# Kernel tuning notes

Measured on AMD Instinct MI355X. Metric: run time of the kernel, lower is better.

The kernel has to match this reference:

```python
import jax, jax.numpy as jnp
import numpy as np

WINDOW_SIZES = [3, 5, 7, 9]
THETA = 1.0
INCLUDE = ['contrast', 'energy', 'entropy', 'homogeneity']
EPS = 1e-6


def _extract_patches(x, w):
    # x: [B, C, H, W] -> [B, C, K=w*w, H, W] with zero padding (matches F.unfold)
    pad = w // 2
    H, W = x.shape[2], x.shape[3]
    xp = jnp.pad(x, ((0, 0), (0, 0), (pad, pad), (pad, pad)))
    shifts = [xp[:, :, i:i + H, j:j + W] for i in range(w) for j in range(w)]
    return jnp.stack(shifts, axis=2)


def _glcm_feats(patches):
    # patches: [B, C, K, H, W]; all reductions over K (axis=2)
    mean = jnp.mean(patches, axis=2, keepdims=True)
    std = jnp.std(patches, axis=2, ddof=1, keepdims=True) + EPS  # torch.std is unbiased
    normed = (patches - mean) / std
    contrast = jnp.mean(normed ** 2, axis=2)
    energy = jnp.mean(patches ** 2, axis=2)
    entropy = -jnp.mean(patches * jnp.log(patches + EPS), axis=2)
    homogeneity = 1.0 / jnp.mean(1.0 + jnp.abs(patches - mean), axis=2)
    return {'contrast': contrast, 'energy': energy,
            'entropy': entropy, 'homogeneity': homogeneity}


def setup_inputs() -> dict:
    key = jax.random.key(0)
    x = jax.random.uniform(key, (2, 3, 512, 512), dtype=jnp.float32)
    return {'x': x}


def reference(x):
    B, C, H, W = x.shape
    per_window = []
    for w in WINDOW_SIZES:
        patches = _extract_patches(x, w)          # [B, C, K, H, W]
        feats = _glcm_feats(patches)
        Ms = []
        for name in ['contrast', 'energy', 'entropy', 'homogeneity']:
            if name in INCLUDE:
                log_feat = jnp.log(feats[name] + EPS)
                Ms.append(jnp.exp(THETA * log_feat - 0.5 * THETA ** 2))
        per_window.append(jnp.stack(Ms, axis=2))  # [B, C, F, H, W]
    out = jnp.concatenate(per_window, axis=2)     # [B, C, nW*F, H, W]
    # channel-major ordering (c outer, then window, then feature) matches the
    # torch module's per-channel loop + final cat along dim=1
    return out.reshape(B, C * out.shape[2], H, W)
```

## Files before the change

### kernel.cpp

```cpp
#include <hip/hip_runtime.h>
#include <math.h>

#define BC 6
#define H_ 512
#define W_ 512
#define HW (H_ * W_)
#define EPS 1e-6f
#define EXPM05 0.60653065971263342f

#define TW 72
#define TH 16
#define XSS 18
#define VHS 72

__global__ __launch_bounds__(256) void texmart_kernel(const float* __restrict__ x,
                                                      float* __restrict__ out) {
    __shared__ float xs[TW][XSS];
    __shared__ float vh[48][VHS];

    const int tx = threadIdx.x, ty = threadIdx.y;
    const int tid = ty * 64 + tx;
    const int bx = blockIdx.x * 64, by = blockIdx.y * 8;
    const int plane = blockIdx.z;
    const float* __restrict__ xp = x + (size_t)plane * HW;

    for (int idx = tid; idx < TW * TH; idx += 256) {
        const int t = idx / TW, c = idx - t * TW;
        const int gy = by + t - 4, gx = bx + c - 4;
        float v = 0.f;
        if (gy >= 0 && gy < H_ && gx >= 0 && gx < W_) v = xp[gy * W_ + gx];
        xs[c][t] = v;
    }
    __syncthreads();

    int uoA[3], ucA[3];
    float s1A[3], s2A[3], slA[3];
#pragma unroll
    for (int i = 0; i < 3; ++i) {
        const int u = tid + i * 256;
        const int uu = (u < 576) ? u : 0;
        const int o = uu / 72, c = uu - o * 72;
        uoA[i] = o; ucA[i] = c;
        const float pc = xs[c][o + 4];
        s1A[i] = pc;
        s2A[i] = pc * pc;
        slA[i] = pc * __logf(pc + EPS);
    }

    float mean[2][4];
    const int gxx = bx + tx;
    float* __restrict__ obase = out + (size_t)plane * 16 * HW + (size_t)by * W_ + gxx;

#pragma unroll
    for (int round = 0; round < 2; ++round) {
        const int Rb = 1 + 2 * round;

#pragma unroll
        for (int i = 0; i < 3; ++i) {
            if (i < 2 || tid < 64) {
                const int o = uoA[i], c = ucA[i];
#pragma unroll
                for (int rr = 0; rr < 2; ++rr) {
                    const int R = Rb + rr;
                    const float plo = xs[c][o + 4 - R];
                    const float phi = xs[c][o + 4 + R];
                    s1A[i] += plo + phi;
                    s2A[i] = __fmaf_rn(plo, plo, __fmaf_rn(phi, phi, s2A[i]));
                    slA[i] += plo * __logf(plo + EPS) + phi * __logf(phi + EPS);
                    vh[(rr * 3 + 0) * 8 + o][c] = s1A[i];
                    vh[(rr * 3 + 1) * 8 + o][c] = s2A[i];
                    vh[(rr * 3 + 2) * 8 + o][c] = slA[i];
                }
            }
        }
        __syncthreads();

#pragma unroll
        for (int rr = 0; rr < 2; ++rr) {
            const int R = Rb + rr;
            const float K = (float)((2 * R + 1) * (2 * R + 1));
            const float invK = 1.f / K;
            const float invKm1 = 1.f / (K - 1.f);
#pragma unroll
            for (int oi = 0; oi < 2; ++oi) {
                const int o = ty * 2 + oi;
                float S1 = 0.f, S2 = 0.f, SL = 0.f;
#pragma unroll
                for (int s = -4; s <= 4; ++s) {
                    if (s >= -R && s <= R) {
                        S1 += vh[(rr * 3 + 0) * 8 + o][tx + 4 + s];
                        S2 += vh[(rr * 3 + 1) * 8 + o][tx + 4 + s];
                        SL += vh[(rr * 3 + 2) * 8 + o][tx + 4 + s];
                    }
                }
                const float m = S1 * invK;
                mean[oi][R - 1] = m;
                float S2c = __fmaf_rn(-S1, m, S2);
                if (S2c < 0.f) S2c = 0.f;
                const float sd = sqrtf(S2c * invKm1) + EPS;
                const float contrast = (S2c * invK) * __frcp_rn(sd * sd);
                const float energy = S2 * invK;
                const float entropy = -SL * invK;

                float* __restrict__ o4 = obase + (size_t)o * W_ + (size_t)(R - 1) * 4 * HW;
                o4[0 * HW] = (contrast + EPS) * EXPM05;
                o4[1 * HW] = (energy + EPS) * EXPM05;
                o4[2 * HW] = (entropy + EPS) * EXPM05;
            }
        }
        if (round == 0) __syncthreads();
    }

    const int ty2 = ty * 2;
    float sa[2][4];
#pragma unroll
    for (int oi = 0; oi < 2; ++oi)
#pragma unroll
        for (int R = 0; R < 4; ++R) sa[oi][R] = 0.f;

#pragma unroll
    for (int dj = 0; dj < 9; ++dj) {
        const int a = dj < 4 ? 4 - dj : dj - 4;
        const float* __restrict__ col = &xs[tx + dj][ty2];
        const float2 u0 = *(const float2*)(col + 0);
        const float2 u1 = *(const float2*)(col + 2);
        const float2 u2 = *(const float2*)(col + 4);
        const float2 u3 = *(const float2*)(col + 6);
        const float2 u4 = *(const float2*)(col + 8);
        const float p[10] = {u0.x, u0.y, u1.x, u1.y, u2.x, u2.y, u3.x, u3.y, u4.x, u4.y};

#pragma unroll
        for (int oi = 0; oi < 2; ++oi) {
#pragma unroll
            for (int k = 0; k < 9; ++k) {
                const int adi = k < 4 ? 4 - k : k - 4;
                const int rm = a > adi ? a : adi;
                const int r0 = rm < 1 ? 1 : rm;
#pragma unroll
                for (int R = 1; R <= 4; ++R) {
                    if (R >= r0) sa[oi][R - 1] += fabsf(p[oi + k] - mean[oi][R - 1]);
                }
            }
        }
    }

#pragma unroll
    for (int oi = 0; oi < 2; ++oi) {
        const int o = ty2 + oi;
#pragma unroll
        for (int R = 1; R <= 4; ++R) {
            const float K = (float)((2 * R + 1) * (2 * R + 1));
            const float homog = __frcp_rn(1.f + sa[oi][R - 1] * (1.f / K));
            obase[(size_t)o * W_ + (size_t)(R - 1) * 4 * HW + 3 * HW] =
                (homog + EPS) * EXPM05;
        }
    }
}

extern "C" void kernel_launch(void* const* d_in, const int* in_sizes, int n_in,
                              void* d_out, int out_size, void* d_ws, size_t ws_size,
                              hipStream_t stream) {
    const float* x = (const float*)d_in[0];
    float* out = (float*)d_out;
    dim3 block(64, 4, 1);
    dim3 grid(W_ / 64, H_ / 8, BC);
    texmart_kernel<<<grid, block, 0, stream>>>(x, out);
}
```

Baseline: 45.52 us.

## Retile to 64x32 blocks with four-column threads, cached logs and sliding sums

Grows each block's tile from 64x8 to 64x32 and gives every thread four adjacent output columns. It precomputes x*log(x) once per tile element into shared memory, so the vertical prefix passes no longer recompute logs, and processes each radius separately with float4 shared loads. The horizontal window sums now slide across the four columns, and all outputs are written as float4 stores. In exchange, shared memory and register pressure rise (per-thread mean and abs-deviation arrays), which may reduce occupancy.

```diff
diff --git a/kernel.cpp b/kernel.cpp
--- a/kernel.cpp
+++ b/kernel.cpp
@@ -8,137 +8,159 @@
 #define EPS 1e-6f
 #define EXPM05 0.60653065971263342f
 
-#define TW 72
-#define TH 16
-#define XSS 18
-#define VHS 72
+#define TCOLS 72
+#define TROWS 40
+#define XST 76
 
 __global__ __launch_bounds__(256) void texmart_kernel(const float* __restrict__ x,
                                                       float* __restrict__ out) {
-    __shared__ float xs[TW][XSS];
-    __shared__ float vh[48][VHS];
+    __shared__ float xs[TROWS][XST];
+    __shared__ float qs[TROWS][XST];
+    __shared__ float vh[3][32][XST];
 
-    const int tx = threadIdx.x, ty = threadIdx.y;
-    const int tid = ty * 64 + tx;
-    const int bx = blockIdx.x * 64, by = blockIdx.y * 8;
+    const int tix = threadIdx.x;
+    const int tiy = threadIdx.y;
+    const int tid = tiy * 16 + tix;
+    const int bx = blockIdx.x * 64, by = blockIdx.y * 32;
     const int plane = blockIdx.z;
     const float* __restrict__ xp = x + (size_t)plane * HW;
 
-    for (int idx = tid; idx < TW * TH; idx += 256) {
-        const int t = idx / TW, c = idx - t * TW;
+    for (int idx = tid; idx < TROWS * TCOLS; idx += 256) {
+        const int t = idx / TCOLS, c = idx - t * TCOLS;
         const int gy = by + t - 4, gx = bx + c - 4;
         float v = 0.f;
         if (gy >= 0 && gy < H_ && gx >= 0 && gx < W_) v = xp[gy * W_ + gx];
-        xs[c][t] = v;
+        xs[t][c] = v;
+        qs[t][c] = v * __logf(v + EPS);
     }
     __syncthreads();
 
+    float s1A[3][4], s2A[3][4], slA[3][4];
     int uoA[3], ucA[3];
-    float s1A[3], s2A[3], slA[3];
 #pragma unroll
     for (int i = 0; i < 3; ++i) {
         const int u = tid + i * 256;
         const int uu = (u < 576) ? u : 0;
-        const int o = uu / 72, c = uu - o * 72;
-        uoA[i] = o; ucA[i] = c;
-        const float pc = xs[c][o + 4];
-        s1A[i] = pc;
-        s2A[i] = pc * pc;
-        slA[i] = pc * __logf(pc + EPS);
+        const int o = uu / 18, cg = uu - (uu / 18) * 18;
+        uoA[i] = o; ucA[i] = 4 * cg;
+        float pc[4], qc[4];
+        *(float4*)pc = *(const float4*)&xs[o + 4][4 * cg];
+        *(float4*)qc = *(const float4*)&qs[o + 4][4 * cg];
+#pragma unroll
+        for (int j = 0; j < 4; ++j) {
+            s1A[i][j] = pc[j];
+            s2A[i][j] = pc[j] * pc[j];
+            slA[i][j] = qc[j];
+        }
     }
 
-    float mean[2][4];
-    const int gxx = bx + tx;
-    float* __restrict__ obase = out + (size_t)plane * 16 * HW + (size_t)by * W_ + gxx;
+    float mean_[2][4][4];
+    const int gx0 = bx + 4 * tix;
+    float* __restrict__ obase = out + (size_t)plane * 16 * HW + (size_t)by * W_ + gx0;
 
 #pragma unroll
-    for (int round = 0; round < 2; ++round) {
-        const int Rb = 1 + 2 * round;
-
+    for (int R = 1; R <= 4; ++R) {
 #pragma unroll
         for (int i = 0; i < 3; ++i) {
             if (i < 2 || tid < 64) {
-                const int o = uoA[i], c = ucA[i];
+                const int o = uoA[i], c4 = ucA[i];
+                float lo[4], hi[4], ql[4], qh[4];
+                *(float4*)lo = *(const float4*)&xs[o + 4 - R][c4];
+                *(float4*)hi = *(const float4*)&xs[o + 4 + R][c4];
+                *(float4*)ql = *(const float4*)&qs[o + 4 - R][c4];
+                *(float4*)qh = *(const float4*)&qs[o + 4 + R][c4];
+                float w1[4], w2[4], wl[4];
 #pragma unroll
-                for (int rr = 0; rr < 2; ++rr) {
-                    const int R = Rb + rr;
-                    const float plo = xs[c][o + 4 - R];
-                    const float phi = xs[c][o + 4 + R];
-                    s1A[i] += plo + phi;
-                    s2A[i] = __fmaf_rn(plo, plo, __fmaf_rn(phi, phi, s2A[i]));
-                    slA[i] += plo * __logf(plo + EPS) + phi * __logf(phi + EPS);
-                    vh[(rr * 3 + 0) * 8 + o][c] = s1A[i];
-                    vh[(rr * 3 + 1) * 8 + o][c] = s2A[i];
-                    vh[(rr * 3 + 2) * 8 + o][c] = slA[i];
+                for (int j = 0; j < 4; ++j) {
+                    s1A[i][j] += lo[j] + hi[j];
+                    s2A[i][j] = __fmaf_rn(lo[j], lo[j], __fmaf_rn(hi[j], hi[j], s2A[i][j]));
+                    slA[i][j] += ql[j] + qh[j];
+                    w1[j] = s1A[i][j]; w2[j] = s2A[i][j]; wl[j] = slA[i][j];
                 }
+                *(float4*)&vh[0][o][c4] = *(float4*)w1;
+                *(float4*)&vh[1][o][c4] = *(float4*)w2;
+                *(float4*)&vh[2][o][c4] = *(float4*)wl;
             }
         }
         __syncthreads();
 
+        const float K = (float)((2 * R + 1) * (2 * R + 1));
+        const float invK = 1.f / K;
+        const float invKm1 = 1.f / (K - 1.f);
 #pragma unroll
-        for (int rr = 0; rr < 2; ++rr) {
-            const int R = Rb + rr;
-            const float K = (float)((2 * R + 1) * (2 * R + 1));
-            const float invK = 1.f / K;
-            const float invKm1 = 1.f / (K - 1.f);
+        for (int oi = 0; oi < 2; ++oi) {
+            const int o = 2 * tiy + oi;
+            float v1[12], v2[12], vl[12];
+            *(float4*)&v1[0] = *(const float4*)&vh[0][o][4 * tix + 0];
+            *(float4*)&v1[4] = *(const float4*)&vh[0][o][4 * tix + 4];
+            *(float4*)&v1[8] = *(const float4*)&vh[0][o][4 * tix + 8];
+            *(float4*)&v2[0] = *(const float4*)&vh[1][o][4 * tix + 0];
+            *(float4*)&v2[4] = *(const float4*)&vh[1][o][4 * tix + 4];
+            *(float4*)&v2[8] = *(const float4*)&vh[1][o][4 * tix + 8];
+            *(float4*)&vl[0] = *(const float4*)&vh[2][o][4 * tix + 0];
+            *(float4*)&vl[4] = *(const float4*)&vh[2][o][4 * tix + 4];
+            *(float4*)&vl[8] = *(const float4*)&vh[2][o][4 * tix + 8];
+
+            float S1 = 0.f, S2 = 0.f, SL = 0.f;
 #pragma unroll
-            for (int oi = 0; oi < 2; ++oi) {
-                const int o = ty * 2 + oi;
-                float S1 = 0.f, S2 = 0.f, SL = 0.f;
+            for (int s = 4 - R; s <= 4 + R; ++s) { S1 += v1[s]; S2 += v2[s]; SL += vl[s]; }
+
+            float fc[4], fe[4], fh[4];
 #pragma unroll
-                for (int s = -4; s <= 4; ++s) {
-                    if (s >= -R && s <= R) {
-                        S1 += vh[(rr * 3 + 0) * 8 + o][tx + 4 + s];
-                        S2 += vh[(rr * 3 + 1) * 8 + o][tx + 4 + s];
-                        SL += vh[(rr * 3 + 2) * 8 + o][tx + 4 + s];
-                    }
+            for (int j = 0; j < 4; ++j) {
+                if (j > 0) {
+                    S1 += v1[j + 4 + R] - v1[j + 3 - R];
+                    S2 += v2[j + 4 + R] - v2[j + 3 - R];
+                    SL += vl[j + 4 + R] - vl[j + 3 - R];
                 }
                 const float m = S1 * invK;
-                mean[oi][R - 1] = m;
+                mean_[oi][R - 1][j] = m;
                 float S2c = __fmaf_rn(-S1, m, S2);
                 if (S2c < 0.f) S2c = 0.f;
                 const float sd = sqrtf(S2c * invKm1) + EPS;
-                const float contrast = (S2c * invK) * __frcp_rn(sd * sd);
-                const float energy = S2 * invK;
-                const float entropy = -SL * invK;
-
-                float* __restrict__ o4 = obase + (size_t)o * W_ + (size_t)(R - 1) * 4 * HW;
-                o4[0 * HW] = (contrast + EPS) * EXPM05;
-                o4[1 * HW] = (energy + EPS) * EXPM05;
-                o4[2 * HW] = (entropy + EPS) * EXPM05;
+                fc[j] = ((S2c * invK) * __frcp_rn(sd * sd) + EPS) * EXPM05;
+                fe[j] = (S2 * invK + EPS) * EXPM05;
+                fh[j] = (-SL * invK + EPS) * EXPM05;
             }
+            float* __restrict__ o4 = obase + (size_t)o * W_ + (size_t)(R - 1) * 4 * HW;
+            *(float4*)&o4[0 * HW] = *(float4*)fc;
+            *(float4*)&o4[1 * HW] = *(float4*)fe;
+            *(float4*)&o4[2 * HW] = *(float4*)fh;
         }
-        if (round == 0) __syncthreads();
+        if (R < 4) __syncthreads();
     }
 
-    const int ty2 = ty * 2;
-    float sa[2][4];
+    float sa[2][4][4];
 #pragma unroll
     for (int oi = 0; oi < 2; ++oi)
 #pragma unroll
-        for (int R = 0; R < 4; ++R) sa[oi][R] = 0.f;
+        for (int R = 0; R < 4; ++R)
+#pragma unroll
+            for (int j = 0; j < 4; ++j) sa[oi][R][j] = 0.f;
 
 #pragma unroll
-    for (int dj = 0; dj < 9; ++dj) {
-        const int a = dj < 4 ? 4 - dj : dj - 4;
-        const float* __restrict__ col = &xs[tx + dj][ty2];
-        const float2 u0 = *(const float2*)(col + 0);
-        const float2 u1 = *(const float2*)(col + 2);
-        const float2 u2 = *(const float2*)(col + 4);
-        const float2 u3 = *(const float2*)(col + 6);
-        const float2 u4 = *(const float2*)(col + 8);
-        const float p[10] = {u0.x, u0.y, u1.x, u1.y, u2.x, u2.y, u3.x, u3.y, u4.x, u4.y};
-
+    for (int r = 0; r < 10; ++r) {
+        float v[12];
+        *(float4*)&v[0] = *(const float4*)&xs[2 * tiy + r][4 * tix + 0];
+        *(float4*)&v[4] = *(const float4*)&xs[2 * tiy + r][4 * tix + 4];
+        *(float4*)&v[8] = *(const float4*)&xs[2 * tiy + r][4 * tix + 8];
 #pragma unroll
         for (int oi = 0; oi < 2; ++oi) {
-#pragma unroll
-            for (int k = 0; k < 9; ++k) {
-                const int adi = k < 4 ? 4 - k : k - 4;
-                const int rm = a > adi ? a : adi;
-                const int r0 = rm < 1 ? 1 : rm;
+            const int dt = r - 4 - oi;
+            if (dt >= -4 && dt <= 4) {
+                const int adt = dt < 0 ? -dt : dt;
+                const int r0 = adt < 1 ? 1 : adt;
 #pragma unroll
                 for (int R = 1; R <= 4; ++R) {
-                    if (R >= r0) sa[oi][R - 1] += fabsf(p[oi + k] - mean[oi][R - 1]);
+                    if (R >= r0) {
+#pragma unroll
+                        for (int j = 0; j < 4; ++j) {
+                            const float m = mean_[oi][R - 1][j];
+#pragma unroll
+                            for (int s = j + 4 - R; s <= j + 4 + R; ++s)
+                                sa[oi][R - 1][j] += fabsf(v[s] - m);
+                        }
+                    }
                 }
             }
         }
@@ -146,13 +168,16 @@
 
 #pragma unroll
     for (int oi = 0; oi < 2; ++oi) {
-        const int o = ty2 + oi;
+        const int o = 2 * tiy + oi;
 #pragma unroll
         for (int R = 1; R <= 4; ++R) {
             const float K = (float)((2 * R + 1) * (2 * R + 1));
-            const float homog = __frcp_rn(1.f + sa[oi][R - 1] * (1.f / K));
-            obase[(size_t)o * W_ + (size_t)(R - 1) * 4 * HW + 3 * HW] =
-                (homog + EPS) * EXPM05;
+            float fh[4];
+#pragma unroll
+            for (int j = 0; j < 4; ++j)
+                fh[j] = (__frcp_rn(1.f + sa[oi][R - 1][j] * (1.f / K)) + EPS) * EXPM05;
+            float* __restrict__ o4 = obase + (size_t)o * W_ + (size_t)(R - 1) * 4 * HW;
+            *(float4*)&o4[3 * HW] = *(float4*)fh;
         }
     }
 }
@@ -162,7 +187,7 @@
                               hipStream_t stream) {
     const float* x = (const float*)d_in[0];
     float* out = (float*)d_out;
-    dim3 block(64, 4, 1);
-    dim3 grid(W_ / 64, H_ / 8, BC);
+    dim3 block(16, 16, 1);
+    dim3 grid(W_ / 64, H_ / 32, BC);
     texmart_kernel<<<grid, block, 0, stream>>>(x, out);
 }
```

New measurement: 48.05 us. 5.6% more time.
